# Performance work log

Hardware: AMD Instinct MI355X
Metric: run time of the kernel (lower is better)

## Reference

```python
import jax, jax.numpy as jnp
import numpy as np

SEQ_LEN, BATCH, INPUT_DIM, HIDDEN_DIM = 2048, 16, 1024, 2048
COMPRESSION_RATIO = 0.5


def setup_inputs() -> dict:
    key = jax.random.key(0)
    ks = jax.random.split(key, 10)
    s_in = 0.02  # xavier-ish scale for (hidden, input) linears
    return {
        "x": jax.random.normal(ks[0], (SEQ_LEN, BATCH, INPUT_DIM), dtype=jnp.float32),
        "A": jax.random.normal(ks[1], (HIDDEN_DIM, HIDDEN_DIM), dtype=jnp.float32) * 0.1 - 0.5,
        "W_B": jax.random.normal(ks[2], (HIDDEN_DIM, INPUT_DIM), dtype=jnp.float32) * s_in,
        "W_C": jax.random.normal(ks[3], (HIDDEN_DIM, INPUT_DIM), dtype=jnp.float32) * s_in,
        "W_delta": jax.random.normal(ks[4], (HIDDEN_DIM, INPUT_DIM), dtype=jnp.float32) * s_in,
        "b_delta": jnp.zeros((HIDDEN_DIM,), dtype=jnp.float32),
        "W_in": jax.random.normal(ks[5], (HIDDEN_DIM, INPUT_DIM), dtype=jnp.float32) * s_in,
        "b_in": jnp.zeros((HIDDEN_DIM,), dtype=jnp.float32),
        "W_comp": jax.random.normal(ks[6], (INPUT_DIM, HIDDEN_DIM), dtype=jnp.float32) * s_in,
        "b_comp": jnp.zeros((INPUT_DIM,), dtype=jnp.float32),
    }


def reference(x, A, W_B, W_C, W_delta, b_delta, W_in, b_in, W_comp, b_comp):
    # x: (S, B, D_in).  A is an unused parameter in the original forward.
    seq_len = x.shape[0]
    compressed_len = max(1, int(seq_len * COMPRESSION_RATIO))
    step = seq_len // compressed_len

    # Batched projections over all timesteps (replaces per-step Linears)
    B_all = jnp.einsum('sbd,hd->sbh', x, W_B)                       # (S, B, H)
    C_all = jnp.einsum('sbd,hd->sbh', x, W_C)                       # (S, B, H)
    delta = jax.nn.softplus(jnp.einsum('sbd,hd->sbh', x, W_delta) + b_delta)
    u = jnp.einsum('sbd,hd->sbh', x, W_in) + b_in + B_all           # x_proj + B_t

    # Gated linear recurrence: h_t = (1 - delta_t) * h_{t-1} + delta_t * u_t
    def step_fn(h, inp):
        d, uu = inp
        h = (1.0 - d) * h + d * uu
        return h, h

    h0 = jnp.zeros((x.shape[1], u.shape[-1]), dtype=x.dtype)
    _, hs = jax.lax.scan(step_fn, h0, (delta, u))                   # (S, B, H)

    y = C_all * hs                                                  # (S, B, H)

    # Output at the last timestep of each window of size `step`
    idx = np.array([min(i + step, seq_len) - 1 for i in range(0, seq_len, step)])
    y_sel = y[idx]                                                  # (S_c, B, H)
    return jnp.einsum('sbh,dh->sbd', y_sel, W_comp) + b_comp        # (S_c, B, D_in)
```

## Files before the change

kernel.cpp:

```cpp
#include <hip/hip_runtime.h>
#include <hip/hip_bf16.h>
#include <cstdio>

#define S_LEN 2048
#define BATCH 16
#define D_INP 1024
#define H_DIM 2048
#define SC    (S_LEN / 2)
#define BH    (BATCH * H_DIM)
#define NC    16
#define CS    (S_LEN / NC)

typedef __bf16 b16;
typedef __bf16 b16x8 __attribute__((ext_vector_type(8)));
typedef __bf16 b16x4 __attribute__((ext_vector_type(4)));
typedef float  f32x4 __attribute__((ext_vector_type(4)));

__device__ __forceinline__ int sw_off(int r, int k8) {
  return r * 32 + ((k8 ^ ((r >> 1) & 3)) << 3);
}

__device__ __forceinline__ void gl2lds16(const b16* g, b16* l) {
  __builtin_amdgcn_global_load_lds(
      (const __attribute__((address_space(1))) void*)g,
      (__attribute__((address_space(3))) void*)l, 16, 0, 0);
}

__device__ __forceinline__ float softplus_fast(float t) {
  float e = __expf(-fabsf(t));
  return fmaxf(t, 0.f) + __logf(1.f + e);
}

__global__ void cvt_x_kernel(const float* __restrict__ in, b16* __restrict__ out, int n4) {
  int i = blockIdx.x * 256 + threadIdx.x;
  if (i >= n4) return;
  float4 v = ((const float4*)in)[i];
  b16x4 o = {(b16)v.x, (b16)v.y, (b16)v.z, (b16)v.w};
  ((b16x4*)out)[i] = o;
}

__global__ void prep_w_kernel(const float* __restrict__ Wd, const float* __restrict__ Win,
                              const float* __restrict__ WB, const float* __restrict__ Wc,
                              const float* __restrict__ Wcp,
                              b16* __restrict__ Wdu, b16* __restrict__ Wcb,
                              b16* __restrict__ Wcpb) {
  const int HD4 = (H_DIM * D_INP) / 4;
  int i = blockIdx.x * 256 + threadIdx.x;
  if (i >= HD4) return;
  float4 a = ((const float4*)Wd)[i];
  float4 b = ((const float4*)Win)[i];
  float4 c = ((const float4*)WB)[i];
  float4 d = ((const float4*)Wc)[i];
  float4 e = ((const float4*)Wcp)[i];
  ((b16x4*)Wdu)[i] = {(b16)a.x, (b16)a.y, (b16)a.z, (b16)a.w};
  ((b16x4*)Wdu)[HD4 + i] = {(b16)(b.x + c.x), (b16)(b.y + c.y), (b16)(b.z + c.z), (b16)(b.w + c.w)};
  ((b16x4*)Wcb)[i] = {(b16)d.x, (b16)d.y, (b16)d.z, (b16)d.w};
  ((b16x4*)Wcpb)[i] = {(b16)e.x, (b16)e.y, (b16)e.z, (b16)e.w};
}

template <int MODE>
__device__ __forceinline__ void stage256(const b16* __restrict__ A, const b16* __restrict__ W,
                                         int K, int k0, b16* buf, int m0, int n0,
                                         int wave, int lane) {
  const int w = wave & 3;
  const bool isB = wave >= 4;
  const int rr = lane >> 2;
  const int gp = lane & 3;
#pragma unroll
  for (int l = 0; l < 4; ++l) {
    const int rbase = w * 64 + l * 16;
    const int r = rbase + rr;
    const int gl = gp ^ ((r >> 1) & 3);
    b16* dst = buf + (isB ? 256 * 32 : 0) + rbase * 32;
    const b16* src;
    if (isB) {
      src = W + (long)(n0 + r) * K + k0 + gl * 8;
    } else {
      long arow = m0 + r;
      if (MODE == 1) arow = 2 * arow - (arow & 15) + 16;
      src = A + arow * (long)K + k0 + gl * 8;
    }
    gl2lds16(src, dst);
  }
}

template <int MODE>
__global__ __launch_bounds__(512, 2) void gemm256(
    const b16* __restrict__ A, const b16* __restrict__ W, int K,
    const float* __restrict__ bias0, const float* __restrict__ bias1,
    const b16* __restrict__ hsel, b16* __restrict__ ob0, b16* __restrict__ ob1,
    float* __restrict__ of) {
  extern __shared__ b16 lds[];
  const int tid  = threadIdx.x;
  const int lane = tid & 63;
  const int wave = tid >> 6;
  const int wm = wave >> 2, wn = wave & 3;
  const int lm = lane & 15;
  const int l8 = lane >> 4;

  const int gx  = gridDim.x;
  const int nwg = gx * gridDim.y;
  const int id0 = blockIdx.y * gx + blockIdx.x;
  const int sw  = (id0 & 7) * (nwg >> 3) + (id0 >> 3);
  const int m0 = (sw / gx) * 256;
  const int n0 = (sw % gx) * 256;

  f32x4 acc[8][4];
#pragma unroll
  for (int i = 0; i < 8; i++)
#pragma unroll
    for (int j = 0; j < 4; j++) acc[i][j] = (f32x4)0.f;

  const int NT = K >> 5;
  stage256<MODE>(A, W, K, 0,  lds + 0 * 16384, m0, n0, wave, lane);
  stage256<MODE>(A, W, K, 32, lds + 1 * 16384, m0, n0, wave, lane);
  stage256<MODE>(A, W, K, 64, lds + 2 * 16384, m0, n0, wave, lane);

  for (int t = 0; t < NT; ++t) {
    if (t + 2 < NT)      asm volatile("s_waitcnt vmcnt(8)" ::: "memory");
    else if (t + 1 < NT) asm volatile("s_waitcnt vmcnt(4)" ::: "memory");
    else                 asm volatile("s_waitcnt vmcnt(0)" ::: "memory");
    __builtin_amdgcn_s_barrier();
    if (t + 3 < NT)
      stage256<MODE>(A, W, K, (t + 3) << 5, lds + (size_t)((t + 3) & 3) * 16384,
                     m0, n0, wave, lane);
    const b16* As = lds + (size_t)(t & 3) * 16384;
    const b16* Bs = As + 256 * 32;
    b16x8 af[8], bfr[4];
#pragma unroll
    for (int i = 0; i < 8; i++) af[i] = *(const b16x8*)(As + sw_off(wm * 128 + i * 16 + lm, l8));
#pragma unroll
    for (int j = 0; j < 4; j++) bfr[j] = *(const b16x8*)(Bs + sw_off(wn * 64 + j * 16 + lm, l8));
    __builtin_amdgcn_s_setprio(1);
#pragma unroll
    for (int i = 0; i < 8; i++)
#pragma unroll
      for (int j = 0; j < 4; j++)
        acc[i][j] = __builtin_amdgcn_mfma_f32_16x16x32_bf16(af[i], bfr[j], acc[i][j], 0, 0, 0);
    __builtin_amdgcn_s_setprio(0);
  }

  if (MODE == 0) {
    const bool is_delta = (n0 < H_DIM);
    const float* bias = is_delta ? bias0 : bias1;
    b16* ob = is_delta ? ob0 : ob1;
    const int nc0 = (n0 & (H_DIM - 1)) + wn * 64 + lm;
    float bv[4];
#pragma unroll
    for (int j = 0; j < 4; j++) bv[j] = bias[nc0 + j * 16];
#pragma unroll
    for (int i = 0; i < 8; i++) {
      const long rb = m0 + wm * 128 + i * 16 + l8 * 4;
      b16* pr = ob + rb * H_DIM + nc0;
      if (is_delta) {
#pragma unroll
        for (int j = 0; j < 4; j++)
#pragma unroll
          for (int rg = 0; rg < 4; ++rg)
            pr[(long)rg * H_DIM + j * 16] = (b16)softplus_fast(acc[i][j][rg] + bv[j]);
      } else {
#pragma unroll
        for (int j = 0; j < 4; j++)
#pragma unroll
          for (int rg = 0; rg < 4; ++rg)
            pr[(long)rg * H_DIM + j * 16] = (b16)(acc[i][j][rg] + bv[j]);
      }
    }
  } else if (MODE == 1) {
    const int nc0 = n0 + wn * 64 + lm;
#pragma unroll
    for (int i = 0; i < 8; i++) {
      const long rb = m0 + wm * 128 + i * 16 + l8 * 4;
      const b16* hp = hsel + rb * H_DIM + nc0;
      b16* pr = ob0 + rb * H_DIM + nc0;
#pragma unroll
      for (int j = 0; j < 4; j++)
#pragma unroll
        for (int rg = 0; rg < 4; ++rg) {
          float hv = (float)hp[(long)rg * H_DIM + j * 16];
          pr[(long)rg * H_DIM + j * 16] = (b16)(acc[i][j][rg] * hv);
        }
    }
  } else {
    const int nc0 = n0 + wn * 64 + lm;
    float bv[4];
#pragma unroll
    for (int j = 0; j < 4; j++) bv[j] = bias0[nc0 + j * 16];
#pragma unroll
    for (int i = 0; i < 8; i++) {
      const long rb = m0 + wm * 128 + i * 16 + l8 * 4;
      float* pr = of + rb * D_INP + nc0;
#pragma unroll
      for (int j = 0; j < 4; j++)
#pragma unroll
        for (int rg = 0; rg < 4; ++rg)
          pr[(long)rg * D_INP + j * 16] = acc[i][j][rg] + bv[j];
    }
  }
}

template <int MODE>
__global__ __launch_bounds__(256, 2) void gemm_bt(
    const b16* __restrict__ A, const b16* __restrict__ W, int K,
    const float* __restrict__ bias0, const float* __restrict__ bias1,
    const b16* __restrict__ hsel, b16* __restrict__ ob0, b16* __restrict__ ob1,
    float* __restrict__ of) {
  __shared__ b16 As[128 * 32];
  __shared__ b16 Bs[128 * 32];
  const int tid  = threadIdx.x;
  const int lane = tid & 63;
  const int wave = tid >> 6;
  const int wr = wave >> 1, wc = wave & 1;
  const int m0 = blockIdx.y * 128;
  const int n0 = blockIdx.x * 128;
  const int lm = lane & 15;
  const int l8 = lane >> 4;
  const int rL  = wave * 16 + (lane >> 2);
  const int k8p = lane & 3;

  f32x4 acc[4][4];
#pragma unroll
  for (int i = 0; i < 4; i++)
#pragma unroll
    for (int j = 0; j < 4; j++) acc[i][j] = (f32x4)0.f;

  for (int k0 = 0; k0 < K; k0 += 32) {
#pragma unroll
    for (int hh = 0; hh < 2; ++hh) {
      const int r = rL + hh * 64;
      const int k8l = k8p ^ ((r >> 1) & 3);
      b16* ldsA = As + (wave * 16 + hh * 64) * 32;
      b16* ldsB = Bs + (wave * 16 + hh * 64) * 32;
      long arow = m0 + r;
      if (MODE == 1) arow = 2 * arow - (arow & 15) + 16;
      gl2lds16(A + arow * (long)K + k0 + k8l * 8, ldsA);
      gl2lds16(W + (long)(n0 + r) * K + k0 + k8l * 8, ldsB);
    }
    __syncthreads();
    b16x8 af[4], bfr[4];
#pragma unroll
    for (int i = 0; i < 4; i++) af[i] = *(const b16x8*)(As + sw_off(wr * 64 + i * 16 + lm, l8));
#pragma unroll
    for (int j = 0; j < 4; j++) bfr[j] = *(const b16x8*)(Bs + sw_off(wc * 64 + j * 16 + lm, l8));
#pragma unroll
    for (int i = 0; i < 4; i++)
#pragma unroll
      for (int j = 0; j < 4; j++)
        acc[i][j] = __builtin_amdgcn_mfma_f32_16x16x32_bf16(af[i], bfr[j], acc[i][j], 0, 0, 0);
    __syncthreads();
  }

  if (MODE == 0) {
    const bool is_delta = (n0 < H_DIM);
    const float* bias = is_delta ? bias0 : bias1;
    b16* ob = is_delta ? ob0 : ob1;
    const int nc0 = (n0 & (H_DIM - 1)) + wc * 64 + lm;
    float bv[4];
#pragma unroll
    for (int j = 0; j < 4; j++) bv[j] = bias[nc0 + j * 16];
#pragma unroll
    for (int i = 0; i < 4; i++) {
      const long rb = m0 + wr * 64 + i * 16 + l8 * 4;
      b16* pr = ob + rb * H_DIM + nc0;
      if (is_delta) {
#pragma unroll
        for (int j = 0; j < 4; j++)
#pragma unroll
          for (int rg = 0; rg < 4; ++rg)
            pr[(long)rg * H_DIM + j * 16] = (b16)softplus_fast(acc[i][j][rg] + bv[j]);
      } else {
#pragma unroll
        for (int j = 0; j < 4; j++)
#pragma unroll
          for (int rg = 0; rg < 4; ++rg)
            pr[(long)rg * H_DIM + j * 16] = (b16)(acc[i][j][rg] + bv[j]);
      }
    }
  } else if (MODE == 1) {
    const int nc0 = n0 + wc * 64 + lm;
#pragma unroll
    for (int i = 0; i < 4; i++) {
      const long rb = m0 + wr * 64 + i * 16 + l8 * 4;
      const b16* hp = hsel + rb * H_DIM + nc0;
      b16* pr = ob0 + rb * H_DIM + nc0;
#pragma unroll
      for (int j = 0; j < 4; j++)
#pragma unroll
        for (int rg = 0; rg < 4; ++rg) {
          float hv = (float)hp[(long)rg * H_DIM + j * 16];
          pr[(long)rg * H_DIM + j * 16] = (b16)(acc[i][j][rg] * hv);
        }
    }
  } else {
    const int nc0 = n0 + wc * 64 + lm;
    float bv[4];
#pragma unroll
    for (int j = 0; j < 4; j++) bv[j] = bias0[nc0 + j * 16];
#pragma unroll
    for (int i = 0; i < 4; i++) {
      const long rb = m0 + wr * 64 + i * 16 + l8 * 4;
      float* pr = of + rb * D_INP + nc0;
#pragma unroll
      for (int j = 0; j < 4; j++)
#pragma unroll
        for (int rg = 0; rg < 4; ++rg)
          pr[(long)rg * D_INP + j * 16] = acc[i][j][rg] + bv[j];
    }
  }
}

__global__ void scan_a_kernel(const b16* __restrict__ dl, const b16* __restrict__ uu,
                              float* __restrict__ P, float* __restrict__ Q) {
  int g = blockIdx.x * 256 + threadIdx.x;
  int c = g >> 15;
  int p = g & (BH - 1);
  const b16* dp = dl + (size_t)c * CS * BH + p;
  const b16* up = uu + (size_t)c * CS * BH + p;
  float h = 0.f, pr = 1.f;
#pragma unroll 4
  for (int s = 0; s < CS; ++s) {
    float d = (float)dp[(size_t)s * BH];
    float u = (float)up[(size_t)s * BH];
    float a = 1.f - d;
    h = a * h + d * u;
    pr *= a;
  }
  P[g] = pr;
  Q[g] = h;
}

__global__ void scan_b_kernel(const float* __restrict__ P, const float* __restrict__ Q,
                              float* __restrict__ Hs) {
  int p = blockIdx.x * 256 + threadIdx.x;
  float h = 0.f;
#pragma unroll
  for (int c = 0; c < NC; ++c) {
    Hs[c * BH + p] = h;
    h = P[c * BH + p] * h + Q[c * BH + p];
  }
}

__global__ void scan_c_kernel(const b16* __restrict__ dl, const b16* __restrict__ uu,
                              const float* __restrict__ Hs, b16* __restrict__ hsel) {
  int g = blockIdx.x * 256 + threadIdx.x;
  int c = g >> 15;
  int p = g & (BH - 1);
  const b16* dp = dl + (size_t)c * CS * BH + p;
  const b16* up = uu + (size_t)c * CS * BH + p;
  b16* hp = hsel + (size_t)(c * (CS / 2)) * BH + p;
  float h = Hs[g];
#pragma unroll 4
  for (int s = 0; s < CS; ++s) {
    float d = (float)dp[(size_t)s * BH];
    float u = (float)up[(size_t)s * BH];
    h = (1.f - d) * h + d * u;
    if (s & 1) hp[(size_t)(s >> 1) * BH] = (b16)h;
  }
}

extern "C" void kernel_launch(void* const* d_in, const int* in_sizes, int n_in,
                              void* d_out, int out_size, void* d_ws, size_t ws_size,
                              hipStream_t stream) {
  const float* x   = (const float*)d_in[0];
  const float* WB  = (const float*)d_in[2];
  const float* Wc  = (const float*)d_in[3];
  const float* Wd  = (const float*)d_in[4];
  const float* bd  = (const float*)d_in[5];
  const float* Win = (const float*)d_in[6];
  const float* bi  = (const float*)d_in[7];
  const float* Wcp = (const float*)d_in[8];
  const float* bc  = (const float*)d_in[9];
  float* out = (float*)d_out;

  char* w = (char*)d_ws;
  size_t off = 0;
  auto alloc = [&](size_t bytes) {
    void* p = w + off;
    off += (bytes + 255) & ~(size_t)255;
    return p;
  };
  b16* xb   = (b16*)alloc((size_t)S_LEN * BATCH * D_INP * 2);
  b16* Wdu  = (b16*)alloc((size_t)2 * H_DIM * D_INP * 2);
  b16* Wcb  = (b16*)alloc((size_t)H_DIM * D_INP * 2);
  b16* Wcpb = (b16*)alloc((size_t)D_INP * H_DIM * 2);
  b16* dbuf = (b16*)alloc((size_t)S_LEN * BH * 2);
  b16* ubuf = (b16*)alloc((size_t)S_LEN * BH * 2);
  b16* hsel = (b16*)alloc((size_t)SC * BH * 2);
  b16* ysel = (b16*)alloc((size_t)SC * BH * 2);
  float* P  = (float*)alloc((size_t)NC * BH * 4);
  float* Q  = (float*)alloc((size_t)NC * BH * 4);
  float* Hs = (float*)alloc((size_t)NC * BH * 4);
  if (off > ws_size) {
    fprintf(stderr, "kernel_launch: ws too small: need %zu have %zu\n", off, ws_size);
    return;
  }

  static int g_big = -1;
  if (g_big < 0) {
    hipError_t e0 = hipFuncSetAttribute(reinterpret_cast<const void*>(&gemm256<0>),
                                        hipFuncAttributeMaxDynamicSharedMemorySize, 131072);
    hipError_t e1 = hipFuncSetAttribute(reinterpret_cast<const void*>(&gemm256<1>),
                                        hipFuncAttributeMaxDynamicSharedMemorySize, 131072);
    hipError_t e2 = hipFuncSetAttribute(reinterpret_cast<const void*>(&gemm256<2>),
                                        hipFuncAttributeMaxDynamicSharedMemorySize, 131072);
    g_big = (e0 == hipSuccess && e1 == hipSuccess && e2 == hipSuccess) ? 1 : 0;
  }

  int n4 = S_LEN * BATCH * D_INP / 4;
  cvt_x_kernel<<<(n4 + 255) / 256, 256, 0, stream>>>(x, xb, n4);
  int hd4 = H_DIM * D_INP / 4;
  prep_w_kernel<<<(hd4 + 255) / 256, 256, 0, stream>>>(Wd, Win, WB, Wc, Wcp, Wdu, Wcb, Wcpb);
  if (g_big) {
    dim3 g1(2 * H_DIM / 256, S_LEN * BATCH / 256);
    gemm256<0><<<g1, 512, 131072, stream>>>(xb, Wdu, D_INP, bd, bi, nullptr, dbuf, ubuf, nullptr);
  } else {
    dim3 g1(2 * H_DIM / 128, S_LEN * BATCH / 128);
    gemm_bt<0><<<g1, 256, 0, stream>>>(xb, Wdu, D_INP, bd, bi, nullptr, dbuf, ubuf, nullptr);
  }
  scan_a_kernel<<<NC * BH / 256, 256, 0, stream>>>(dbuf, ubuf, P, Q);
  scan_b_kernel<<<BH / 256, 256, 0, stream>>>(P, Q, Hs);
  scan_c_kernel<<<NC * BH / 256, 256, 0, stream>>>(dbuf, ubuf, Hs, hsel);
  if (g_big) {
    dim3 g2(H_DIM / 256, SC * BATCH / 256);
    gemm256<1><<<g2, 512, 131072, stream>>>(xb, Wcb, D_INP, nullptr, nullptr, hsel, ysel, nullptr, nullptr);
  } else {
    dim3 g2(H_DIM / 128, SC * BATCH / 128);
    gemm_bt<1><<<g2, 256, 0, stream>>>(xb, Wcb, D_INP, nullptr, nullptr, hsel, ysel, nullptr, nullptr);
  }
  if (g_big) {
    dim3 g3(D_INP / 256, SC * BATCH / 256);
    gemm256<2><<<g3, 512, 131072, stream>>>(ysel, Wcpb, H_DIM, bc, nullptr, nullptr, nullptr, nullptr, out);
  } else {
    dim3 g3(D_INP / 128, SC * BATCH / 128);
    gemm_bt<2><<<g3, 256, 0, stream>>>(ysel, Wcpb, H_DIM, bc, nullptr, nullptr, nullptr, nullptr, out);
  }
}
```

Baseline: 841.1 us.

## Restructure 256x256 GEMM mainloop into 8-phase ping-pong schedule with split prefetch

```diff
diff --git a/kernel.cpp b/kernel.cpp
--- a/kernel.cpp
+++ b/kernel.cpp
@@ -58,34 +58,29 @@
   ((b16x4*)Wcpb)[i] = {(b16)e.x, (b16)e.y, (b16)e.z, (b16)e.w};
 }
 
+#define AH0 0
+#define AH1 8192
+#define BH0 16384
+#define BH1 24576
+
 template <int MODE>
-__device__ __forceinline__ void stage256(const b16* __restrict__ A, const b16* __restrict__ W,
-                                         int K, int k0, b16* buf, int m0, int n0,
-                                         int wave, int lane) {
-  const int w = wave & 3;
-  const bool isB = wave >= 4;
-  const int rr = lane >> 2;
-  const int gp = lane & 3;
-#pragma unroll
-  for (int l = 0; l < 4; ++l) {
-    const int rbase = w * 64 + l * 16;
-    const int r = rbase + rr;
-    const int gl = gp ^ ((r >> 1) & 3);
-    b16* dst = buf + (isB ? 256 * 32 : 0) + rbase * 32;
-    const b16* src;
-    if (isB) {
-      src = W + (long)(n0 + r) * K + k0 + gl * 8;
-    } else {
-      long arow = m0 + r;
-      if (MODE == 1) arow = 2 * arow - (arow & 15) + 16;
-      src = A + arow * (long)K + k0 + gl * 8;
-    }
-    gl2lds16(src, dst);
+__device__ __forceinline__ void stage_half(const b16* __restrict__ G, int ldg,
+                                           int base_row, int kcol, b16* half_base,
+                                           int wave, int lane, bool isA) {
+#pragma unroll
+  for (int q = 0; q < 2; ++q) {
+    const int rbase = q * 128 + wave * 16;
+    const int r = rbase + (lane >> 2);
+    const int p = lane & 3;
+    const int gl = p ^ ((r >> 1) & 3);
+    long grow = base_row + r;
+    if (MODE == 1 && isA) grow = 2 * grow - (grow & 15) + 16;
+    gl2lds16(G + grow * (long)ldg + kcol + gl * 8, half_base + rbase * 32);
   }
 }
 
 template <int MODE>
-__global__ __launch_bounds__(512, 2) void gemm256(
+__global__ __launch_bounds__(512, 2) void gemm8p(
     const b16* __restrict__ A, const b16* __restrict__ W, int K,
     const float* __restrict__ bias0, const float* __restrict__ bias1,
     const b16* __restrict__ hsel, b16* __restrict__ ob0, b16* __restrict__ ob1,
@@ -111,33 +106,98 @@
 #pragma unroll
     for (int j = 0; j < 4; j++) acc[i][j] = (f32x4)0.f;
 
-  const int NT = K >> 5;
-  stage256<MODE>(A, W, K, 0,  lds + 0 * 16384, m0, n0, wave, lane);
-  stage256<MODE>(A, W, K, 32, lds + 1 * 16384, m0, n0, wave, lane);
-  stage256<MODE>(A, W, K, 64, lds + 2 * 16384, m0, n0, wave, lane);
+  const int NT = K >> 6;
+
+  {
+    b16* B0 = lds;
+    stage_half<MODE>(A, K, m0, 0,  B0 + AH0, wave, lane, true);
+    stage_half<MODE>(W, K, n0, 0,  B0 + BH0, wave, lane, false);
+    stage_half<MODE>(A, K, m0, 32, B0 + AH1, wave, lane, true);
+    stage_half<MODE>(W, K, n0, 32, B0 + BH1, wave, lane, false);
+    asm volatile("s_waitcnt vmcnt(4)" ::: "memory");
+    __builtin_amdgcn_s_barrier();
+  }
 
   for (int t = 0; t < NT; ++t) {
-    if (t + 2 < NT)      asm volatile("s_waitcnt vmcnt(8)" ::: "memory");
-    else if (t + 1 < NT) asm volatile("s_waitcnt vmcnt(4)" ::: "memory");
-    else                 asm volatile("s_waitcnt vmcnt(0)" ::: "memory");
-    __builtin_amdgcn_s_barrier();
-    if (t + 3 < NT)
-      stage256<MODE>(A, W, K, (t + 3) << 5, lds + (size_t)((t + 3) & 3) * 16384,
-                     m0, n0, wave, lane);
-    const b16* As = lds + (size_t)(t & 3) * 16384;
-    const b16* Bs = As + 256 * 32;
-    b16x8 af[8], bfr[4];
-#pragma unroll
-    for (int i = 0; i < 8; i++) af[i] = *(const b16x8*)(As + sw_off(wm * 128 + i * 16 + lm, l8));
-#pragma unroll
-    for (int j = 0; j < 4; j++) bfr[j] = *(const b16x8*)(Bs + sw_off(wn * 64 + j * 16 + lm, l8));
+    b16* const C = lds + ((t & 1) << 15);
+    b16* const N = lds + (((t + 1) & 1) << 15);
+    const int kn = (t + 1) << 6;
+    const bool pf = (t + 1 < NT);
+    b16x8 a[8], bb0, bb1;
+
+#pragma unroll
+    for (int i = 0; i < 8; i++)
+      a[i] = *(const b16x8*)(C + AH0 + sw_off(wm * 128 + i * 16 + lm, l8));
+    bb0 = *(const b16x8*)(C + BH0 + sw_off(wn * 64 + 0 + lm, l8));
+    bb1 = *(const b16x8*)(C + BH0 + sw_off(wn * 64 + 16 + lm, l8));
+    if (pf) stage_half<MODE>(A, K, m0, kn, N + AH0, wave, lane, true);
+    __builtin_amdgcn_s_barrier();
+    asm volatile("s_waitcnt lgkmcnt(0)" ::: "memory");
+    __builtin_amdgcn_sched_barrier(0);
     __builtin_amdgcn_s_setprio(1);
 #pragma unroll
+    for (int i = 0; i < 8; i++) {
+      acc[i][0] = __builtin_amdgcn_mfma_f32_16x16x32_bf16(a[i], bb0, acc[i][0], 0, 0, 0);
+      acc[i][1] = __builtin_amdgcn_mfma_f32_16x16x32_bf16(a[i], bb1, acc[i][1], 0, 0, 0);
+    }
+    __builtin_amdgcn_s_setprio(0);
+    __builtin_amdgcn_s_barrier();
+
+    bb0 = *(const b16x8*)(C + BH0 + sw_off(wn * 64 + 32 + lm, l8));
+    bb1 = *(const b16x8*)(C + BH0 + sw_off(wn * 64 + 48 + lm, l8));
+    if (pf) {
+      stage_half<MODE>(W, K, n0, kn, N + BH0, wave, lane, false);
+      asm volatile("s_waitcnt vmcnt(4)" ::: "memory");
+    } else {
+      asm volatile("s_waitcnt vmcnt(0)" ::: "memory");
+    }
+    __builtin_amdgcn_s_barrier();
+    asm volatile("s_waitcnt lgkmcnt(0)" ::: "memory");
+    __builtin_amdgcn_sched_barrier(0);
+    __builtin_amdgcn_s_setprio(1);
+#pragma unroll
+    for (int i = 0; i < 8; i++) {
+      acc[i][2] = __builtin_amdgcn_mfma_f32_16x16x32_bf16(a[i], bb0, acc[i][2], 0, 0, 0);
+      acc[i][3] = __builtin_amdgcn_mfma_f32_16x16x32_bf16(a[i], bb1, acc[i][3], 0, 0, 0);
+    }
+    __builtin_amdgcn_s_setprio(0);
+    __builtin_amdgcn_s_barrier();
+
+#pragma unroll
     for (int i = 0; i < 8; i++)
-#pragma unroll
-      for (int j = 0; j < 4; j++)
-        acc[i][j] = __builtin_amdgcn_mfma_f32_16x16x32_bf16(af[i], bfr[j], acc[i][j], 0, 0, 0);
+      a[i] = *(const b16x8*)(C + AH1 + sw_off(wm * 128 + i * 16 + lm, l8));
+    bb0 = *(const b16x8*)(C + BH1 + sw_off(wn * 64 + 0 + lm, l8));
+    bb1 = *(const b16x8*)(C + BH1 + sw_off(wn * 64 + 16 + lm, l8));
+    if (pf) stage_half<MODE>(A, K, m0, kn + 32, N + AH1, wave, lane, true);
+    __builtin_amdgcn_s_barrier();
+    asm volatile("s_waitcnt lgkmcnt(0)" ::: "memory");
+    __builtin_amdgcn_sched_barrier(0);
+    __builtin_amdgcn_s_setprio(1);
+#pragma unroll
+    for (int i = 0; i < 8; i++) {
+      acc[i][0] = __builtin_amdgcn_mfma_f32_16x16x32_bf16(a[i], bb0, acc[i][0], 0, 0, 0);
+      acc[i][1] = __builtin_amdgcn_mfma_f32_16x16x32_bf16(a[i], bb1, acc[i][1], 0, 0, 0);
+    }
     __builtin_amdgcn_s_setprio(0);
+    __builtin_amdgcn_s_barrier();
+
+    bb0 = *(const b16x8*)(C + BH1 + sw_off(wn * 64 + 32 + lm, l8));
+    bb1 = *(const b16x8*)(C + BH1 + sw_off(wn * 64 + 48 + lm, l8));
+    if (pf) {
+      stage_half<MODE>(W, K, n0, kn + 32, N + BH1, wave, lane, false);
+      asm volatile("s_waitcnt vmcnt(4)" ::: "memory");
+    }
+    __builtin_amdgcn_s_barrier();
+    asm volatile("s_waitcnt lgkmcnt(0)" ::: "memory");
+    __builtin_amdgcn_sched_barrier(0);
+    __builtin_amdgcn_s_setprio(1);
+#pragma unroll
+    for (int i = 0; i < 8; i++) {
+      acc[i][2] = __builtin_amdgcn_mfma_f32_16x16x32_bf16(a[i], bb0, acc[i][2], 0, 0, 0);
+      acc[i][3] = __builtin_amdgcn_mfma_f32_16x16x32_bf16(a[i], bb1, acc[i][3], 0, 0, 0);
+    }
+    __builtin_amdgcn_s_setprio(0);
+    __builtin_amdgcn_s_barrier();
   }
 
   if (MODE == 0) {
@@ -197,6 +257,10 @@
           pr[(long)rg * D_INP + j * 16] = acc[i][j][rg] + bv[j];
     }
   }
+}
+
+__device__ __forceinline__ int sw_off128(int r, int k8) {
+  return r * 32 + ((k8 ^ ((r >> 1) & 3)) << 3);
 }
 
 template <int MODE>
@@ -239,9 +303,9 @@
     __syncthreads();
     b16x8 af[4], bfr[4];
 #pragma unroll
-    for (int i = 0; i < 4; i++) af[i] = *(const b16x8*)(As + sw_off(wr * 64 + i * 16 + lm, l8));
-#pragma unroll
-    for (int j = 0; j < 4; j++) bfr[j] = *(const b16x8*)(Bs + sw_off(wc * 64 + j * 16 + lm, l8));
+    for (int i = 0; i < 4; i++) af[i] = *(const b16x8*)(As + sw_off128(wr * 64 + i * 16 + lm, l8));
+#pragma unroll
+    for (int j = 0; j < 4; j++) bfr[j] = *(const b16x8*)(Bs + sw_off128(wc * 64 + j * 16 + lm, l8));
 #pragma unroll
     for (int i = 0; i < 4; i++)
 #pragma unroll
@@ -397,11 +461,11 @@
 
   static int g_big = -1;
   if (g_big < 0) {
-    hipError_t e0 = hipFuncSetAttribute(reinterpret_cast<const void*>(&gemm256<0>),
+    hipError_t e0 = hipFuncSetAttribute(reinterpret_cast<const void*>(&gemm8p<0>),
                                         hipFuncAttributeMaxDynamicSharedMemorySize, 131072);
-    hipError_t e1 = hipFuncSetAttribute(reinterpret_cast<const void*>(&gemm256<1>),
+    hipError_t e1 = hipFuncSetAttribute(reinterpret_cast<const void*>(&gemm8p<1>),
                                         hipFuncAttributeMaxDynamicSharedMemorySize, 131072);
-    hipError_t e2 = hipFuncSetAttribute(reinterpret_cast<const void*>(&gemm256<2>),
+    hipError_t e2 = hipFuncSetAttribute(reinterpret_cast<const void*>(&gemm8p<2>),
                                         hipFuncAttributeMaxDynamicSharedMemorySize, 131072);
     g_big = (e0 == hipSuccess && e1 == hipSuccess && e2 == hipSuccess) ? 1 : 0;
   }
@@ -412,7 +476,7 @@
   prep_w_kernel<<<(hd4 + 255) / 256, 256, 0, stream>>>(Wd, Win, WB, Wc, Wcp, Wdu, Wcb, Wcpb);
   if (g_big) {
     dim3 g1(2 * H_DIM / 256, S_LEN * BATCH / 256);
-    gemm256<0><<<g1, 512, 131072, stream>>>(xb, Wdu, D_INP, bd, bi, nullptr, dbuf, ubuf, nullptr);
+    gemm8p<0><<<g1, 512, 131072, stream>>>(xb, Wdu, D_INP, bd, bi, nullptr, dbuf, ubuf, nullptr);
   } else {
     dim3 g1(2 * H_DIM / 128, S_LEN * BATCH / 128);
     gemm_bt<0><<<g1, 256, 0, stream>>>(xb, Wdu, D_INP, bd, bi, nullptr, dbuf, ubuf, nullptr);
@@ -422,14 +486,14 @@
   scan_c_kernel<<<NC * BH / 256, 256, 0, stream>>>(dbuf, ubuf, Hs, hsel);
   if (g_big) {
     dim3 g2(H_DIM / 256, SC * BATCH / 256);
-    gemm256<1><<<g2, 512, 131072, stream>>>(xb, Wcb, D_INP, nullptr, nullptr, hsel, ysel, nullptr, nullptr);
+    gemm8p<1><<<g2, 512, 131072, stream>>>(xb, Wcb, D_INP, nullptr, nullptr, hsel, ysel, nullptr, nullptr);
   } else {
     dim3 g2(H_DIM / 128, SC * BATCH / 128);
     gemm_bt<1><<<g2, 256, 0, stream>>>(xb, Wcb, D_INP, nullptr, nullptr, hsel, ysel, nullptr, nullptr);
   }
   if (g_big) {
     dim3 g3(D_INP / 256, SC * BATCH / 256);
-    gemm256<2><<<g3, 512, 131072, stream>>>(ysel, Wcpb, H_DIM, bc, nullptr, nullptr, nullptr, nullptr, out);
+    gemm8p<2><<<g3, 512, 131072, stream>>>(ysel, Wcpb, H_DIM, bc, nullptr, nullptr, nullptr, nullptr, out);
   } else {
     dim3 g3(D_INP / 128, SC * BATCH / 128);
     gemm_bt<2><<<g3, 256, 0, stream>>>(ysel, Wcpb, H_DIM, bc, nullptr, nullptr, nullptr, nullptr, out);
```

New measurement: 811.7 us. 3.5% less time.
